# Optimization experiments

Hardware: AMD Instinct MI355X
Metric: run time of the kernel (lower is better)

Reference implementation:

```python
import jax, jax.numpy as jnp
import numpy as np
from jax import lax

RADIUS = 0.3
NSAMPLE = 16
NPOINT = 1024
NH = 1   # num_heading_bin
NS = 18  # num_size_cluster
EPS = 1e-5  # torch BatchNorm eps


def _bn(x, g, b, m, v):
    # eval-mode batchnorm over the last (channel) axis
    return (x - m) * (g / jnp.sqrt(v + EPS)) + b


def _fps(xyz, npoint):
    # furthest point sampling; xyz: (B,K,3) -> (B,npoint) int32 indices
    B, K, _ = xyz.shape
    def body(carry, _):
        dists, far = carry
        cur = jnp.take_along_axis(xyz, far[:, None, None], axis=1)  # (B,1,3)
        d = jnp.sum((xyz - cur) ** 2, -1)                           # (B,K)
        dists = jnp.minimum(dists, d)
        nxt = jnp.argmax(dists, -1).astype(jnp.int32)
        return (dists, nxt), far
    init = (jnp.full((B, K), 1e10, xyz.dtype), jnp.zeros((B,), jnp.int32))
    _, inds = lax.scan(body, init, None, length=npoint)
    return jnp.swapaxes(inds, 0, 1)  # (B, npoint)


def _ball_query(xyz, new_xyz):
    # first-NSAMPLE points within RADIUS of each center, pad with first hit
    K = xyz.shape[1]
    d2 = jnp.sum((new_xyz[:, :, None, :] - xyz[:, None, :, :]) ** 2, -1)  # (B,S,K)
    mask = d2 < RADIUS ** 2
    idx = jnp.where(mask, jnp.arange(K, dtype=jnp.int32)[None, None, :], K)
    idx = jnp.sort(idx, -1)[..., :NSAMPLE]
    first = idx[..., :1]
    idx = jnp.where(idx == K, first, idx)
    idx = jnp.where(idx == K, 0, idx)  # degenerate: no neighbor at all
    return idx  # (B,S,NSAMPLE)


def setup_inputs() -> dict:
    key = jax.random.key(0)
    ks = jax.random.split(key, 32)
    inp = {}
    inp['xyz'] = jax.random.normal(ks[0], (8, 8192, 3), jnp.float32)
    inp['features'] = jax.random.normal(ks[1], (8, 256, 8192), jnp.float32)
    i = 2
    # shared MLP: 259 -> 128 -> 128 -> 128 (conv2d 1x1, no bias, then BN)
    for l, (o, c) in enumerate([(128, 259), (128, 128), (128, 128)]):
        inp[f'mlp_w{l}'] = jax.random.normal(ks[i], (o, c), jnp.float32) * 0.1; i += 1
        inp[f'mlp_g{l}'] = jnp.ones((o,), jnp.float32)
        inp[f'mlp_b{l}'] = jnp.zeros((o,), jnp.float32)
        inp[f'mlp_m{l}'] = jax.random.normal(ks[i], (o,), jnp.float32) * 0.01; i += 1
        inp[f'mlp_v{l}'] = jax.random.uniform(ks[i], (o,), jnp.float32, 0.5, 1.5); i += 1
    # box head convs (conv1d k=1)
    for nm, (o, c) in [('c1', (128, 128)), ('c2', (128, 128)), ('c3', (97, 128))]:
        inp[f'{nm}_w'] = jax.random.normal(ks[i], (o, c), jnp.float32) * 0.1; i += 1
        inp[f'{nm}_b'] = jnp.zeros((o,), jnp.float32)
    for nm in ['bn1', 'bn2']:
        inp[f'{nm}_g'] = jnp.ones((128,), jnp.float32)
        inp[f'{nm}_b'] = jnp.zeros((128,), jnp.float32)
        inp[f'{nm}_m'] = jax.random.normal(ks[i], (128,), jnp.float32) * 0.01; i += 1
        inp[f'{nm}_v'] = jax.random.uniform(ks[i], (128,), jnp.float32, 0.5, 1.5); i += 1
    inp['mean_size_arr'] = jax.random.uniform(ks[i], (NS, 3), jnp.float32, 0.3, 2.0)
    return inp


def reference(xyz, features,
              mlp_w0, mlp_g0, mlp_b0, mlp_m0, mlp_v0,
              mlp_w1, mlp_g1, mlp_b1, mlp_m1, mlp_v1,
              mlp_w2, mlp_g2, mlp_b2, mlp_m2, mlp_v2,
              c1_w, c1_b, bn1_g, bn1_b, bn1_m, bn1_v,
              c2_w, c2_b, bn2_g, bn2_b, bn2_m, bn2_v,
              c3_w, c3_b, mean_size_arr):
    B = xyz.shape[0]
    # --- vote aggregation: FPS + ball query + group + shared MLP + maxpool ---
    fps_inds = _fps(xyz, NPOINT)
    new_xyz = jnp.take_along_axis(xyz, fps_inds[..., None], axis=1)  # (B,S,3)
    idx = _ball_query(xyz, new_xyz)                                  # (B,S,n)
    gather = jax.vmap(lambda a, i: a[i])
    g_xyz = (gather(xyz, idx) - new_xyz[:, :, None, :]) / RADIUS     # normalize_xyz
    g_f = gather(jnp.swapaxes(features, 1, 2), idx)                  # (B,S,n,256)
    h = jnp.concatenate([g_xyz, g_f], -1)                            # (B,S,n,259)
    for w, g, b, m, v in ((mlp_w0, mlp_g0, mlp_b0, mlp_m0, mlp_v0),
                          (mlp_w1, mlp_g1, mlp_b1, mlp_m1, mlp_v1),
                          (mlp_w2, mlp_g2, mlp_b2, mlp_m2, mlp_v2)):
        h = jax.nn.relu(_bn(jnp.einsum('bsnc,oc->bsno', h, w), g, b, m, v))
    feat = jnp.max(h, axis=2)                                        # (B,S,128)
    # --- box head (conv1d k=1 == per-point linear) ---
    net = jax.nn.relu(_bn(jnp.einsum('bsc,oc->bso', feat, c1_w) + c1_b,
                          bn1_g, bn1_b, bn1_m, bn1_v))
    net = jax.nn.relu(_bn(jnp.einsum('bsc,oc->bso', net, c2_w) + c2_b,
                          bn2_g, bn2_b, bn2_m, bn2_v))
    net = jnp.einsum('bsc,oc->bso', net, c3_w) + c3_b                # (B,S,97)
    # --- decode_scores ---
    obj = net[..., 0:2]
    center = new_xyz + net[..., 2:5]
    hs = net[..., 5:5 + NH]
    hr = net[..., 5 + NH:5 + 2 * NH] * (np.pi / NH)
    ss = net[..., 5 + 2 * NH:5 + 2 * NH + NS]
    srn = net[..., 5 + 2 * NH + NS:5 + 2 * NH + 4 * NS].reshape(B, NPOINT, NS, 3)
    sr = (srn * mean_size_arr[None, None]).reshape(B, NPOINT, NS * 3)
    sem = net[..., 5 + 2 * NH + 4 * NS:]
    return jnp.concatenate([obj, center, hs, hr, ss, sr, sem], -1)   # (B,S,97)
```

## Files before the change

### kernel.cpp

```cpp
#include <hip/hip_runtime.h>
#include <cstdint>
#include <cstddef>

#define BATCH   8
#define KPTS    8192
#define NPT     1024
#define NSAMP   16
#define RAD2    0.09f

typedef float f32x2 __attribute__((ext_vector_type(2)));
typedef float f32x4 __attribute__((ext_vector_type(4)));
typedef short s16x4 __attribute__((ext_vector_type(4)));
typedef short s16x8 __attribute__((ext_vector_type(8)));

__device__ __forceinline__ unsigned short f2bf(float x) {
    unsigned u = __float_as_uint(x);
    return (unsigned short)((u + 0x7fffu + ((u >> 16) & 1u)) >> 16);
}

template <int CTRL>
__device__ __forceinline__ float dppmaxf(float v) {
    int o = __builtin_amdgcn_update_dpp(0, __float_as_int(v), CTRL, 0xf, 0xf, true);
    return fmaxf(v, __int_as_float(o));
}

__global__ __launch_bounds__(256, 1) void fps_f0_kernel(
    const float* __restrict__ xyz, float* __restrict__ new_xyz,
    const float* __restrict__ feats, const float* __restrict__ w0,
    float* __restrict__ f0out) {
    __shared__ float xs[KPTS], ys[KPTS], zs[KPTS];
    __shared__ unsigned long long slot3[3];
    __shared__ int   hist[NPT];
    __shared__ float As[16 * 64];
    __shared__ float Bs[16 * 130];

    const int tid = threadIdx.x;

    if (blockIdx.x >= 8) {
        const int bid = blockIdx.x - 8;
        const int b   = bid >> 7;
        const int p0  = (bid & 127) << 6;
        const int rb  = (tid >> 4) << 2;
        const int ob  = tid & 15;
        const float* fb = feats + (size_t)b * 256 * KPTS;

        float acc[4][8];
#pragma unroll
        for (int r = 0; r < 4; ++r)
#pragma unroll
            for (int c = 0; c < 8; ++c) acc[r][c] = 0.f;

        for (int k0 = 0; k0 < 256; k0 += 16) {
#pragma unroll
            for (int i = 0; i < 4; ++i) {
                int e = tid + (i << 8);
                int kk = e >> 6, pc = e & 63;
                As[kk * 64 + pc] = fb[(size_t)(k0 + kk) * KPTS + p0 + pc];
            }
#pragma unroll
            for (int i = 0; i < 8; ++i) {
                int e = tid + (i << 8);
                int o = e >> 4, kk = e & 15;
                Bs[kk * 130 + o] = w0[o * 259 + 3 + k0 + kk];
            }
            __syncthreads();
#pragma unroll
            for (int kk = 0; kk < 16; ++kk) {
                float a[4], wvv[8];
#pragma unroll
                for (int r = 0; r < 4; ++r) a[r] = As[kk * 64 + rb + r];
#pragma unroll
                for (int c = 0; c < 8; ++c) wvv[c] = Bs[kk * 130 + ob + (c << 4)];
#pragma unroll
                for (int r = 0; r < 4; ++r)
#pragma unroll
                    for (int c = 0; c < 8; ++c) acc[r][c] = fmaf(a[r], wvv[c], acc[r][c]);
            }
            __syncthreads();
        }
#pragma unroll
        for (int r = 0; r < 4; ++r) {
            float* outp = f0out + ((size_t)b * KPTS + p0 + rb + r) * 128 + ob;
#pragma unroll
            for (int c = 0; c < 8; ++c) outp[c << 4] = acc[r][c];
        }
        return;
    }

    {
#pragma clang fp contract(off)
        const int b = blockIdx.x;
        const float* xb = xyz + (size_t)b * KPTS * 3;

        for (int i = tid; i < KPTS; i += 256) {
            xs[i] = xb[i * 3 + 0];
            ys[i] = xb[i * 3 + 1];
            zs[i] = xb[i * 3 + 2];
        }
        if (tid < 3) slot3[tid] = 0ull;
        __syncthreads();

        const int base = tid << 5;
        f32x2 px[16], py[16], pz[16], dmn[16];
#pragma unroll
        for (int j = 0; j < 16; ++j) {
            int i0 = base + (j << 1);
            px[j] = (f32x2){xs[i0], xs[i0 + 1]};
            py[j] = (f32x2){ys[i0], ys[i0 + 1]};
            pz[j] = (f32x2){zs[i0], zs[i0 + 1]};
            dmn[j] = (f32x2){1e10f, 1e10f};
        }

        const int lane = tid & 63;
        int far = 0;
        int cur = 0, nxt = 1;
        for (int it = 0; it < NPT; ++it) {
            if (tid == 0) { hist[it] = far; slot3[nxt] = 0ull; }
            const float cx = xs[far], cy = ys[far], cz = zs[far];
            const f32x2 cx2 = (f32x2){cx, cx};
            const f32x2 cy2 = (f32x2){cy, cy};
            const f32x2 cz2 = (f32x2){cz, cz};

            f32x2 mm = (f32x2){-1.0f, -1.0f};
#pragma unroll
            for (int j = 0; j < 16; ++j) {
                f32x2 dx = px[j] - cx2;
                f32x2 dy = py[j] - cy2;
                f32x2 dz = pz[j] - cz2;
                f32x2 d  = (dx * dx + dy * dy) + dz * dz;
                f32x2 nd = __builtin_elementwise_min(dmn[j], d);
                dmn[j] = nd;
                mm = __builtin_elementwise_max(mm, nd);
            }
            float lmax = fmaxf(mm.x, mm.y);

            int ci = 0x7fffffff;
#pragma unroll
            for (int j = 0; j < 16; ++j) {
                if (dmn[j].x == lmax) ci = min(ci, base + (j << 1));
                if (dmn[j].y == lmax) ci = min(ci, base + (j << 1) + 1);
            }

            float wm = lmax;
            wm = dppmaxf<0x111>(wm);
            wm = dppmaxf<0x112>(wm);
            wm = dppmaxf<0x114>(wm);
            wm = dppmaxf<0x118>(wm);
            wm = dppmaxf<0x142>(wm);
            wm = dppmaxf<0x143>(wm);
            float wmax = __int_as_float(
                __builtin_amdgcn_readlane(__float_as_int(wm), 63));

            unsigned long long mk = __ballot(lmax == wmax);
            int wl = (int)__builtin_ctzll(mk);
            int cw = __builtin_amdgcn_readlane(ci, wl);

            if (lane == 0) {
                unsigned long long pk =
                    ((unsigned long long)__float_as_uint(wmax) << 32)
                    | (unsigned)(8191 - cw);
                atomicMax(&slot3[cur], pk);
            }
            __syncthreads();

            unsigned long long g = slot3[cur];
            far = 8191 - (int)(unsigned)(g & 0xffffffffull);
            cur = nxt;
            nxt = (nxt == 2) ? 0 : nxt + 1;
        }

        for (int i = tid; i < NPT; i += 256) {
            int idx = hist[i];
            float* o = new_xyz + ((size_t)b * NPT + i) * 3;
            o[0] = xs[idx]; o[1] = ys[idx]; o[2] = zs[idx];
        }
    }
}

__global__ __launch_bounds__(256) void ballq_kernel(const float* __restrict__ xyz,
                                                    const float* __restrict__ new_xyz,
                                                    int* __restrict__ idxout) {
    const int tid  = threadIdx.x;
    const int lane = tid & 63;
    const int q    = (blockIdx.x << 2) + (tid >> 6);
    const int b    = q >> 10;
    const float* xb = xyz + (size_t)b * KPTS * 3;
    const float qx = new_xyz[q * 3 + 0];
    const float qy = new_xyz[q * 3 + 1];
    const float qz = new_xyz[q * 3 + 2];
    int* op = idxout + q * NSAMP;

    int total = 0;
    int first_p = 0;
    for (int c = 0; c < KPTS / 64; ++c) {
        int p = (c << 6) + lane;
        float pxv = xb[p * 3 + 0], pyv = xb[p * 3 + 1], pzv = xb[p * 3 + 2];
        float dx = __fsub_rn(qx, pxv), dy = __fsub_rn(qy, pyv), dz = __fsub_rn(qz, pzv);
        float d2 = __fadd_rn(__fadd_rn(__fmul_rn(dx, dx), __fmul_rn(dy, dy)),
                             __fmul_rn(dz, dz));
        bool pred = d2 < RAD2;
        unsigned long long mask = __ballot(pred);
        if (total == 0 && mask != 0ull) first_p = (c << 6) + (int)__builtin_ctzll(mask);
        if (pred) {
            int rank = (int)__popcll(mask & ((1ull << lane) - 1ull));
            int slot = total + rank;
            if (slot < NSAMP) op[slot] = p;
        }
        total += (int)__popcll(mask);
        if (total >= NSAMP) break;
    }
    if (total < NSAMP && lane >= total && lane < NSAMP) op[lane] = first_p;
}

#define HB 136

__global__ __launch_bounds__(256) void mlp_kernel(
    const float* __restrict__ f0, const int* __restrict__ idxw,
    const float* __restrict__ xyz, const float* __restrict__ new_xyz,
    const float* __restrict__ w0,
    const float* __restrict__ g0, const float* __restrict__ b0,
    const float* __restrict__ m0, const float* __restrict__ v0,
    const float* __restrict__ w1,
    const float* __restrict__ g1, const float* __restrict__ b1a,
    const float* __restrict__ m1, const float* __restrict__ v1,
    const float* __restrict__ w2,
    const float* __restrict__ g2, const float* __restrict__ b2a,
    const float* __restrict__ m2, const float* __restrict__ v2,
    float* __restrict__ featout) {
    const int tid = threadIdx.x;
    const int q0  = blockIdx.x << 2;
    const int b   = q0 >> 10;

    __shared__ __align__(16) unsigned short hbf[64 * HB];
    __shared__ __align__(16) unsigned short Wsh[128 * HB];
    __shared__ float gx[64], gy[64], gz[64];
    __shared__ int   pidx[64];
    __shared__ float s0[128], t0[128], wxs[128], wys[128], wzs[128];
    __shared__ float s1[128], t1[128], s2[128], t2[128];

    if (tid < 64) pidx[tid] = idxw[(q0 + (tid >> 4)) * NSAMP + (tid & 15)];
    if (tid < 128) {
        float sc = g0[tid] / sqrtf(v0[tid] + 1e-5f);
        s0[tid] = sc; t0[tid] = b0[tid] - m0[tid] * sc;
        sc = g1[tid] / sqrtf(v1[tid] + 1e-5f);
        s1[tid] = sc; t1[tid] = b1a[tid] - m1[tid] * sc;
        sc = g2[tid] / sqrtf(v2[tid] + 1e-5f);
        s2[tid] = sc; t2[tid] = b2a[tid] - m2[tid] * sc;
        wxs[tid] = w0[tid * 259 + 0];
        wys[tid] = w0[tid * 259 + 1];
        wzs[tid] = w0[tid * 259 + 2];
    }
    __syncthreads();
    if (tid < 64) {
        int p = pidx[tid];
        int q = q0 + (tid >> 4);
        const float* pp = xyz + ((size_t)b * KPTS + p) * 3;
        const float* nq = new_xyz + (size_t)q * 3;
        gx[tid] = (pp[0] - nq[0]) / 0.3f;
        gy[tid] = (pp[1] - nq[1]) / 0.3f;
        gz[tid] = (pp[2] - nq[2]) / 0.3f;
    }
    __syncthreads();

#pragma unroll 2
    for (int i = 0; i < 8; ++i) {
        int e = tid + (i << 8);
        int row = e >> 5, o = (e & 31) << 2;
        int p = pidx[row];
        float4 v4 = *(const float4*)(f0 + ((size_t)b * KPTS + p) * 128 + o);
        float gxr = gx[row], gyr = gy[row], gzr = gz[row];
        float r0 = fmaf(wzs[o + 0], gzr, fmaf(wys[o + 0], gyr, fmaf(wxs[o + 0], gxr, v4.x)));
        float r1 = fmaf(wzs[o + 1], gzr, fmaf(wys[o + 1], gyr, fmaf(wxs[o + 1], gxr, v4.y)));
        float r2 = fmaf(wzs[o + 2], gzr, fmaf(wys[o + 2], gyr, fmaf(wxs[o + 2], gxr, v4.z)));
        float r3 = fmaf(wzs[o + 3], gzr, fmaf(wys[o + 3], gyr, fmaf(wxs[o + 3], gxr, v4.w)));
        s16x4 c4;
        c4.x = (short)f2bf(fmaxf(fmaf(r0, s0[o + 0], t0[o + 0]), 0.f));
        c4.y = (short)f2bf(fmaxf(fmaf(r1, s0[o + 1], t0[o + 1]), 0.f));
        c4.z = (short)f2bf(fmaxf(fmaf(r2, s0[o + 2], t0[o + 2]), 0.f));
        c4.w = (short)f2bf(fmaxf(fmaf(r3, s0[o + 3], t0[o + 3]), 0.f));
        *(s16x4*)&hbf[row * HB + o] = c4;
    }
#pragma unroll 4
    for (int i = 0; i < 16; ++i) {
        int e = tid + (i << 8);
        int o = e >> 5;
        int kt = (e & 31) << 2;
        float4 w4 = *(const float4*)(w1 + o * 128 + kt);
        s16x4 c4 = { (short)f2bf(w4.x), (short)f2bf(w4.y),
                     (short)f2bf(w4.z), (short)f2bf(w4.w) };
        *(s16x4*)&Wsh[o * HB + kt] = c4;
    }
    __syncthreads();

    const int w    = tid >> 6;
    const int lane = tid & 63;
    const int l15  = lane & 15;
    const int quad = lane >> 4;
    const int wrow = w << 4;

    f32x4 acc[8];
#pragma unroll
    for (int t = 0; t < 8; ++t) acc[t] = (f32x4){0.f, 0.f, 0.f, 0.f};
#pragma unroll
    for (int k0 = 0; k0 < 128; k0 += 32) {
        s16x8 a = *(const s16x8*)&hbf[(wrow + l15) * HB + k0 + (quad << 3)];
#pragma unroll
        for (int t = 0; t < 8; ++t) {
            s16x8 bf = *(const s16x8*)&Wsh[((t << 4) + l15) * HB + k0 + (quad << 3)];
            acc[t] = __builtin_amdgcn_mfma_f32_16x16x32_bf16(a, bf, acc[t], 0, 0, 0);
        }
    }
    __syncthreads();

#pragma unroll
    for (int t = 0; t < 8; ++t) {
        int o = (t << 4) + l15;
        float ss = s1[o], tt = t1[o];
#pragma unroll
        for (int r = 0; r < 4; ++r) {
            float v = fmaxf(fmaf(acc[t][r], ss, tt), 0.f);
            hbf[(wrow + (quad << 2) + r) * HB + o] = f2bf(v);
        }
    }
#pragma unroll 4
    for (int i = 0; i < 16; ++i) {
        int e = tid + (i << 8);
        int o = e >> 5;
        int kt = (e & 31) << 2;
        float4 w4 = *(const float4*)(w2 + o * 128 + kt);
        s16x4 c4 = { (short)f2bf(w4.x), (short)f2bf(w4.y),
                     (short)f2bf(w4.z), (short)f2bf(w4.w) };
        *(s16x4*)&Wsh[o * HB + kt] = c4;
    }
    __syncthreads();

#pragma unroll
    for (int t = 0; t < 8; ++t) acc[t] = (f32x4){0.f, 0.f, 0.f, 0.f};
#pragma unroll
    for (int k0 = 0; k0 < 128; k0 += 32) {
        s16x8 a = *(const s16x8*)&hbf[(wrow + l15) * HB + k0 + (quad << 3)];
#pragma unroll
        for (int t = 0; t < 8; ++t) {
            s16x8 bf = *(const s16x8*)&Wsh[((t << 4) + l15) * HB + k0 + (quad << 3)];
            acc[t] = __builtin_amdgcn_mfma_f32_16x16x32_bf16(a, bf, acc[t], 0, 0, 0);
        }
    }

#pragma unroll
    for (int t = 0; t < 8; ++t) {
        int o = (t << 4) + l15;
        float ss = s2[o], tt = t2[o];
        float m0v = fmaxf(fmaf(acc[t][0], ss, tt), 0.f);
        float m1v = fmaxf(fmaf(acc[t][1], ss, tt), 0.f);
        float m2v = fmaxf(fmaf(acc[t][2], ss, tt), 0.f);
        float m3v = fmaxf(fmaf(acc[t][3], ss, tt), 0.f);
        float m = fmaxf(fmaxf(m0v, m1v), fmaxf(m2v, m3v));
        m = fmaxf(m, __shfl_xor(m, 16));
        m = fmaxf(m, __shfl_xor(m, 32));
        if (quad == 0)
            featout[(size_t)(q0 + w) * 128 + o] = m;
    }
}

__global__ __launch_bounds__(256) void head_kernel(
    const float* __restrict__ feat, const float* __restrict__ new_xyz,
    const float* __restrict__ c1w, const float* __restrict__ c1b,
    const float* __restrict__ c2w, const float* __restrict__ c2b,
    const float* __restrict__ c3w, const float* __restrict__ c3b,
    const float* __restrict__ bg1, const float* __restrict__ bb1,
    const float* __restrict__ bm1, const float* __restrict__ bv1,
    const float* __restrict__ bg2, const float* __restrict__ bb2,
    const float* __restrict__ bm2, const float* __restrict__ bv2,
    const float* __restrict__ msz, float* __restrict__ out) {
    const int tid = threadIdx.x;
    const int q0  = blockIdx.x << 3;
    __shared__ float fs[8][128], n1[8][128], n2[8][128];
    __shared__ float s1[128], t1[128], s2[128], t2[128], ms[54];

#pragma unroll
    for (int i = 0; i < 4; ++i) {
        int e = tid + (i << 8);
        fs[e >> 7][e & 127] = feat[(size_t)q0 * 128 + e];
    }
    if (tid < 128) {
        float sc = bg1[tid] / sqrtf(bv1[tid] + 1e-5f);
        s1[tid] = sc; t1[tid] = bb1[tid] - bm1[tid] * sc;
        sc = bg2[tid] / sqrtf(bv2[tid] + 1e-5f);
        s2[tid] = sc; t2[tid] = bb2[tid] - bm2[tid] * sc;
    }
    if (tid < 54) ms[tid] = msz[tid];
    __syncthreads();

    const int o    = tid & 127;
    const int half = tid >> 7;

    {
        float a[4];
#pragma unroll
        for (int j = 0; j < 4; ++j) a[j] = c1b[o];
        const float* wr = c1w + o * 128;
        for (int k = 0; k < 128; k += 4) {
            float4 w4 = *(const float4*)(wr + k);
#pragma unroll
            for (int j = 0; j < 4; ++j) {
                int qq = half * 4 + j;
                a[j] = fmaf(fs[qq][k + 0], w4.x, a[j]);
                a[j] = fmaf(fs[qq][k + 1], w4.y, a[j]);
                a[j] = fmaf(fs[qq][k + 2], w4.z, a[j]);
                a[j] = fmaf(fs[qq][k + 3], w4.w, a[j]);
            }
        }
#pragma unroll
        for (int j = 0; j < 4; ++j)
            n1[half * 4 + j][o] = fmaxf(fmaf(a[j], s1[o], t1[o]), 0.f);
    }
    __syncthreads();
    {
        float a[4];
#pragma unroll
        for (int j = 0; j < 4; ++j) a[j] = c2b[o];
        const float* wr = c2w + o * 128;
        for (int k = 0; k < 128; k += 4) {
            float4 w4 = *(const float4*)(wr + k);
#pragma unroll
            for (int j = 0; j < 4; ++j) {
                int qq = half * 4 + j;
                a[j] = fmaf(n1[qq][k + 0], w4.x, a[j]);
                a[j] = fmaf(n1[qq][k + 1], w4.y, a[j]);
                a[j] = fmaf(n1[qq][k + 2], w4.z, a[j]);
                a[j] = fmaf(n1[qq][k + 3], w4.w, a[j]);
            }
        }
#pragma unroll
        for (int j = 0; j < 4; ++j)
            n2[half * 4 + j][o] = fmaxf(fmaf(a[j], s2[o], t2[o]), 0.f);
    }
    __syncthreads();
    if (o < 97) {
        float a[4];
#pragma unroll
        for (int j = 0; j < 4; ++j) a[j] = c3b[o];
        const float* wr = c3w + o * 128;
        for (int k = 0; k < 128; k += 4) {
            float4 w4 = *(const float4*)(wr + k);
#pragma unroll
            for (int j = 0; j < 4; ++j) {
                int qq = half * 4 + j;
                a[j] = fmaf(n2[qq][k + 0], w4.x, a[j]);
                a[j] = fmaf(n2[qq][k + 1], w4.y, a[j]);
                a[j] = fmaf(n2[qq][k + 2], w4.z, a[j]);
                a[j] = fmaf(n2[qq][k + 3], w4.w, a[j]);
            }
        }
#pragma unroll
        for (int j = 0; j < 4; ++j) {
            int q = q0 + half * 4 + j;
            float v = a[j];
            if (o >= 2 && o < 5) v += new_xyz[(size_t)q * 3 + (o - 2)];
            else if (o == 6) v *= 3.14159265358979323846f;
            else if (o >= 25 && o < 79) v *= ms[o - 25];
            out[(size_t)q * 97 + o] = v;
        }
    }
}

extern "C" void kernel_launch(void* const* d_in, const int* in_sizes, int n_in,
                              void* d_out, int out_size, void* d_ws, size_t ws_size,
                              hipStream_t stream) {
    const float* xyz      = (const float*)d_in[0];
    const float* features = (const float*)d_in[1];
    const float* w0  = (const float*)d_in[2];
    const float* g0  = (const float*)d_in[3];
    const float* b0  = (const float*)d_in[4];
    const float* m0  = (const float*)d_in[5];
    const float* v0  = (const float*)d_in[6];
    const float* w1  = (const float*)d_in[7];
    const float* g1  = (const float*)d_in[8];
    const float* b1  = (const float*)d_in[9];
    const float* m1  = (const float*)d_in[10];
    const float* v1  = (const float*)d_in[11];
    const float* w2  = (const float*)d_in[12];
    const float* g2  = (const float*)d_in[13];
    const float* b2  = (const float*)d_in[14];
    const float* m2  = (const float*)d_in[15];
    const float* v2  = (const float*)d_in[16];
    const float* c1w = (const float*)d_in[17];
    const float* c1b = (const float*)d_in[18];
    const float* c2w = (const float*)d_in[19];
    const float* c2b = (const float*)d_in[20];
    const float* c3w = (const float*)d_in[21];
    const float* c3b = (const float*)d_in[22];
    const float* bg1 = (const float*)d_in[23];
    const float* bb1 = (const float*)d_in[24];
    const float* bm1 = (const float*)d_in[25];
    const float* bv1 = (const float*)d_in[26];
    const float* bg2 = (const float*)d_in[27];
    const float* bb2 = (const float*)d_in[28];
    const float* bm2 = (const float*)d_in[29];
    const float* bv2 = (const float*)d_in[30];
    const float* msz = (const float*)d_in[31];

    float* F0   = (float*)d_ws;
    float* feat = F0 + (size_t)BATCH * KPTS * 128;
    int*   idxw = (int*)(feat + (size_t)BATCH * NPT * 128);
    float* nxyz = (float*)(idxw + (size_t)BATCH * NPT * NSAMP);
    float* outp = (float*)d_out;

    fps_f0_kernel<<<8 + BATCH * (KPTS / 64), 256, 0, stream>>>(
        xyz, nxyz, features, w0, F0);
    ballq_kernel<<<BATCH * NPT / 4, 256, 0, stream>>>(xyz, nxyz, idxw);
    mlp_kernel  <<<BATCH * NPT / 4, 256, 0, stream>>>(
        F0, idxw, xyz, nxyz, w0, g0, b0, m0, v0,
        w1, g1, b1, m1, v1, w2, g2, b2, m2, v2, feat);
    head_kernel <<<BATCH * NPT / 8, 256, 0, stream>>>(
        feat, nxyz, c1w, c1b, c2w, c2b, c3w, c3b,
        bg1, bb1, bm1, bv1, bg2, bb2, bm2, bv2, msz, outp);
}
```

Baseline: 1.233 ms.

## Fuse FPS, feature GEMM, ball query and MLP into persistent kernel with counters

Merges the FPS, first-layer feature GEMM, ball query and shared-MLP kernels into one persistent kernel of 256 blocks. Eight blocks run FPS and publish sampled centers in chunks of 32 through global atomic counters. The other 248 blocks first compute the feature GEMM, then start ball query and MLP for each group of centers as soon as those centers are published. This overlaps the serial FPS with the MLP work and removes kernel-launch gaps and the ball-query index round trip through memory. The cost is spin-wait polling, a shared-memory union, and reliance on all 256 blocks being resident at once to avoid deadlock.

```diff
diff --git a/kernel.cpp b/kernel.cpp
--- a/kernel.cpp
+++ b/kernel.cpp
@@ -7,6 +7,8 @@
 #define NPT     1024
 #define NSAMP   16
 #define RAD2    0.09f
+#define HB      136
+#define NWORK   248
 
 typedef float f32x2 __attribute__((ext_vector_type(2)));
 typedef float f32x4 __attribute__((ext_vector_type(4)));
@@ -24,80 +26,62 @@
     return fmaxf(v, __int_as_float(o));
 }
 
-__global__ __launch_bounds__(256, 1) void fps_f0_kernel(
+__device__ __forceinline__ int aload(int* p) {
+    return __hip_atomic_load(p, __ATOMIC_ACQUIRE, __HIP_MEMORY_SCOPE_AGENT);
+}
+__device__ __forceinline__ void abump(int* p, int v) {
+    __hip_atomic_fetch_add(p, v, __ATOMIC_RELEASE, __HIP_MEMORY_SCOPE_AGENT);
+}
+
+union __align__(16) SM {
+    struct {
+        float xs[KPTS], ys[KPTS], zs[KPTS];
+        unsigned long long slot3[3];
+        int hist[NPT];
+    } fps;
+    struct {
+        float As[16 * 64];
+        float Bs[16 * 130];
+    } gemm;
+    struct {
+        unsigned short W1[128 * HB];
+        unsigned short W2[128 * HB];
+        unsigned short hbf[64 * HB];
+        float gx[64], gy[64], gz[64];
+        int   pidx[64];
+        float s0[128], t0[128], wxs[128], wys[128], wzs[128];
+        float s1[128], t1[128], s2[128], t2[128];
+    } mlp;
+};
+
+__global__ __launch_bounds__(256, 1) void mega_kernel(
     const float* __restrict__ xyz, float* __restrict__ new_xyz,
     const float* __restrict__ feats, const float* __restrict__ w0,
-    float* __restrict__ f0out) {
-    __shared__ float xs[KPTS], ys[KPTS], zs[KPTS];
-    __shared__ unsigned long long slot3[3];
-    __shared__ int   hist[NPT];
-    __shared__ float As[16 * 64];
-    __shared__ float Bs[16 * 130];
-
+    float* __restrict__ f0out,
+    const float* __restrict__ g0, const float* __restrict__ b0,
+    const float* __restrict__ m0, const float* __restrict__ v0,
+    const float* __restrict__ w1,
+    const float* __restrict__ g1, const float* __restrict__ b1a,
+    const float* __restrict__ m1, const float* __restrict__ v1,
+    const float* __restrict__ w2,
+    const float* __restrict__ g2, const float* __restrict__ b2a,
+    const float* __restrict__ m2, const float* __restrict__ v2,
+    float* __restrict__ featout, int* __restrict__ cnt) {
+    __shared__ SM sm;
     const int tid = threadIdx.x;
-
-    if (blockIdx.x >= 8) {
-        const int bid = blockIdx.x - 8;
-        const int b   = bid >> 7;
-        const int p0  = (bid & 127) << 6;
-        const int rb  = (tid >> 4) << 2;
-        const int ob  = tid & 15;
-        const float* fb = feats + (size_t)b * 256 * KPTS;
-
-        float acc[4][8];
-#pragma unroll
-        for (int r = 0; r < 4; ++r)
-#pragma unroll
-            for (int c = 0; c < 8; ++c) acc[r][c] = 0.f;
-
-        for (int k0 = 0; k0 < 256; k0 += 16) {
-#pragma unroll
-            for (int i = 0; i < 4; ++i) {
-                int e = tid + (i << 8);
-                int kk = e >> 6, pc = e & 63;
-                As[kk * 64 + pc] = fb[(size_t)(k0 + kk) * KPTS + p0 + pc];
-            }
-#pragma unroll
-            for (int i = 0; i < 8; ++i) {
-                int e = tid + (i << 8);
-                int o = e >> 4, kk = e & 15;
-                Bs[kk * 130 + o] = w0[o * 259 + 3 + k0 + kk];
-            }
-            __syncthreads();
-#pragma unroll
-            for (int kk = 0; kk < 16; ++kk) {
-                float a[4], wvv[8];
-#pragma unroll
-                for (int r = 0; r < 4; ++r) a[r] = As[kk * 64 + rb + r];
-#pragma unroll
-                for (int c = 0; c < 8; ++c) wvv[c] = Bs[kk * 130 + ob + (c << 4)];
-#pragma unroll
-                for (int r = 0; r < 4; ++r)
-#pragma unroll
-                    for (int c = 0; c < 8; ++c) acc[r][c] = fmaf(a[r], wvv[c], acc[r][c]);
-            }
-            __syncthreads();
-        }
-#pragma unroll
-        for (int r = 0; r < 4; ++r) {
-            float* outp = f0out + ((size_t)b * KPTS + p0 + rb + r) * 128 + ob;
-#pragma unroll
-            for (int c = 0; c < 8; ++c) outp[c << 4] = acc[r][c];
-        }
-        return;
-    }
-
-    {
+    const int bid = blockIdx.x;
+
+    if (bid < 8) {
 #pragma clang fp contract(off)
-        const int b = blockIdx.x;
+        const int b = bid;
         const float* xb = xyz + (size_t)b * KPTS * 3;
 
         for (int i = tid; i < KPTS; i += 256) {
-            xs[i] = xb[i * 3 + 0];
-            ys[i] = xb[i * 3 + 1];
-            zs[i] = xb[i * 3 + 2];
-        }
-        if (tid < 3) slot3[tid] = 0ull;
+            sm.fps.xs[i] = xb[i * 3 + 0];
+            sm.fps.ys[i] = xb[i * 3 + 1];
+            sm.fps.zs[i] = xb[i * 3 + 2];
+        }
+        if (tid < 3) sm.fps.slot3[tid] = 0ull;
         __syncthreads();
 
         const int base = tid << 5;
@@ -105,9 +89,9 @@
 #pragma unroll
         for (int j = 0; j < 16; ++j) {
             int i0 = base + (j << 1);
-            px[j] = (f32x2){xs[i0], xs[i0 + 1]};
-            py[j] = (f32x2){ys[i0], ys[i0 + 1]};
-            pz[j] = (f32x2){zs[i0], zs[i0 + 1]};
+            px[j] = (f32x2){sm.fps.xs[i0], sm.fps.xs[i0 + 1]};
+            py[j] = (f32x2){sm.fps.ys[i0], sm.fps.ys[i0 + 1]};
+            pz[j] = (f32x2){sm.fps.zs[i0], sm.fps.zs[i0 + 1]};
             dmn[j] = (f32x2){1e10f, 1e10f};
         }
 
@@ -115,8 +99,8 @@
         int far = 0;
         int cur = 0, nxt = 1;
         for (int it = 0; it < NPT; ++it) {
-            if (tid == 0) { hist[it] = far; slot3[nxt] = 0ull; }
-            const float cx = xs[far], cy = ys[far], cz = zs[far];
+            if (tid == 0) { sm.fps.hist[it] = far; sm.fps.slot3[nxt] = 0ull; }
+            const float cx = sm.fps.xs[far], cy = sm.fps.ys[far], cz = sm.fps.zs[far];
             const f32x2 cx2 = (f32x2){cx, cx};
             const f32x2 cy2 = (f32x2){cy, cy};
             const f32x2 cz2 = (f32x2){cz, cz};
@@ -159,206 +143,249 @@
                 unsigned long long pk =
                     ((unsigned long long)__float_as_uint(wmax) << 32)
                     | (unsigned)(8191 - cw);
-                atomicMax(&slot3[cur], pk);
+                atomicMax(&sm.fps.slot3[cur], pk);
             }
             __syncthreads();
 
-            unsigned long long g = slot3[cur];
+            unsigned long long g = sm.fps.slot3[cur];
             far = 8191 - (int)(unsigned)(g & 0xffffffffull);
             cur = nxt;
             nxt = (nxt == 2) ? 0 : nxt + 1;
-        }
-
-        for (int i = tid; i < NPT; i += 256) {
-            int idx = hist[i];
-            float* o = new_xyz + ((size_t)b * NPT + i) * 3;
-            o[0] = xs[idx]; o[1] = ys[idx]; o[2] = zs[idx];
-        }
-    }
-}
-
-__global__ __launch_bounds__(256) void ballq_kernel(const float* __restrict__ xyz,
-                                                    const float* __restrict__ new_xyz,
-                                                    int* __restrict__ idxout) {
-    const int tid  = threadIdx.x;
-    const int lane = tid & 63;
-    const int q    = (blockIdx.x << 2) + (tid >> 6);
-    const int b    = q >> 10;
-    const float* xb = xyz + (size_t)b * KPTS * 3;
-    const float qx = new_xyz[q * 3 + 0];
-    const float qy = new_xyz[q * 3 + 1];
-    const float qz = new_xyz[q * 3 + 2];
-    int* op = idxout + q * NSAMP;
-
-    int total = 0;
-    int first_p = 0;
-    for (int c = 0; c < KPTS / 64; ++c) {
-        int p = (c << 6) + lane;
-        float pxv = xb[p * 3 + 0], pyv = xb[p * 3 + 1], pzv = xb[p * 3 + 2];
-        float dx = __fsub_rn(qx, pxv), dy = __fsub_rn(qy, pyv), dz = __fsub_rn(qz, pzv);
-        float d2 = __fadd_rn(__fadd_rn(__fmul_rn(dx, dx), __fmul_rn(dy, dy)),
-                             __fmul_rn(dz, dz));
-        bool pred = d2 < RAD2;
-        unsigned long long mask = __ballot(pred);
-        if (total == 0 && mask != 0ull) first_p = (c << 6) + (int)__builtin_ctzll(mask);
-        if (pred) {
-            int rank = (int)__popcll(mask & ((1ull << lane) - 1ull));
-            int slot = total + rank;
-            if (slot < NSAMP) op[slot] = p;
-        }
-        total += (int)__popcll(mask);
-        if (total >= NSAMP) break;
-    }
-    if (total < NSAMP && lane >= total && lane < NSAMP) op[lane] = first_p;
-}
-
-#define HB 136
-
-__global__ __launch_bounds__(256) void mlp_kernel(
-    const float* __restrict__ f0, const int* __restrict__ idxw,
-    const float* __restrict__ xyz, const float* __restrict__ new_xyz,
-    const float* __restrict__ w0,
-    const float* __restrict__ g0, const float* __restrict__ b0,
-    const float* __restrict__ m0, const float* __restrict__ v0,
-    const float* __restrict__ w1,
-    const float* __restrict__ g1, const float* __restrict__ b1a,
-    const float* __restrict__ m1, const float* __restrict__ v1,
-    const float* __restrict__ w2,
-    const float* __restrict__ g2, const float* __restrict__ b2a,
-    const float* __restrict__ m2, const float* __restrict__ v2,
-    float* __restrict__ featout) {
-    const int tid = threadIdx.x;
-    const int q0  = blockIdx.x << 2;
-    const int b   = q0 >> 10;
-
-    __shared__ __align__(16) unsigned short hbf[64 * HB];
-    __shared__ __align__(16) unsigned short Wsh[128 * HB];
-    __shared__ float gx[64], gy[64], gz[64];
-    __shared__ int   pidx[64];
-    __shared__ float s0[128], t0[128], wxs[128], wys[128], wzs[128];
-    __shared__ float s1[128], t1[128], s2[128], t2[128];
-
-    if (tid < 64) pidx[tid] = idxw[(q0 + (tid >> 4)) * NSAMP + (tid & 15)];
+
+            if ((it & 31) == 31) {
+                if (tid < 128) {
+                    int c = tid & 3;
+                    if (c < 3) {
+                        int i = (it - 31) + (tid >> 2);
+                        int idx = sm.fps.hist[i];
+                        float v = (c == 0) ? sm.fps.xs[idx]
+                                 : (c == 1) ? sm.fps.ys[idx] : sm.fps.zs[idx];
+                        new_xyz[((size_t)b * NPT + i) * 3 + c] = v;
+                    }
+                }
+                __threadfence();
+                __syncthreads();
+                if (tid == 0) abump(&cnt[b], 32);
+            }
+        }
+        return;
+    }
+
+    const int wk = bid - 8;
+
+    {
+        const int rb = (tid >> 4) << 2;
+        const int ob = tid & 15;
+        for (int t = wk; t < 1024; t += NWORK) {
+            const int b  = t >> 7;
+            const int p0 = (t & 127) << 6;
+            const float* fb = feats + (size_t)b * 256 * KPTS;
+
+            float acc[4][8];
+#pragma unroll
+            for (int r = 0; r < 4; ++r)
+#pragma unroll
+                for (int c = 0; c < 8; ++c) acc[r][c] = 0.f;
+
+            for (int k0 = 0; k0 < 256; k0 += 16) {
+#pragma unroll
+                for (int i = 0; i < 4; ++i) {
+                    int e = tid + (i << 8);
+                    int kk = e >> 6, pc = e & 63;
+                    sm.gemm.As[kk * 64 + pc] = fb[(size_t)(k0 + kk) * KPTS + p0 + pc];
+                }
+#pragma unroll
+                for (int i = 0; i < 8; ++i) {
+                    int e = tid + (i << 8);
+                    int o = e >> 4, kk = e & 15;
+                    sm.gemm.Bs[kk * 130 + o] = w0[o * 259 + 3 + k0 + kk];
+                }
+                __syncthreads();
+#pragma unroll
+                for (int kk = 0; kk < 16; ++kk) {
+                    float a[4], wvv[8];
+#pragma unroll
+                    for (int r = 0; r < 4; ++r) a[r] = sm.gemm.As[kk * 64 + rb + r];
+#pragma unroll
+                    for (int c = 0; c < 8; ++c) wvv[c] = sm.gemm.Bs[kk * 130 + ob + (c << 4)];
+#pragma unroll
+                    for (int r = 0; r < 4; ++r)
+#pragma unroll
+                        for (int c = 0; c < 8; ++c) acc[r][c] = fmaf(a[r], wvv[c], acc[r][c]);
+                }
+                __syncthreads();
+            }
+#pragma unroll
+            for (int r = 0; r < 4; ++r) {
+                float* outp = f0out + ((size_t)b * KPTS + p0 + rb + r) * 128 + ob;
+#pragma unroll
+                for (int c = 0; c < 8; ++c) outp[c << 4] = acc[r][c];
+            }
+        }
+        __threadfence();
+        __syncthreads();
+        if (tid == 0) abump(&cnt[8], 1);
+    }
+
     if (tid < 128) {
         float sc = g0[tid] / sqrtf(v0[tid] + 1e-5f);
-        s0[tid] = sc; t0[tid] = b0[tid] - m0[tid] * sc;
+        sm.mlp.s0[tid] = sc; sm.mlp.t0[tid] = b0[tid] - m0[tid] * sc;
         sc = g1[tid] / sqrtf(v1[tid] + 1e-5f);
-        s1[tid] = sc; t1[tid] = b1a[tid] - m1[tid] * sc;
+        sm.mlp.s1[tid] = sc; sm.mlp.t1[tid] = b1a[tid] - m1[tid] * sc;
         sc = g2[tid] / sqrtf(v2[tid] + 1e-5f);
-        s2[tid] = sc; t2[tid] = b2a[tid] - m2[tid] * sc;
-        wxs[tid] = w0[tid * 259 + 0];
-        wys[tid] = w0[tid * 259 + 1];
-        wzs[tid] = w0[tid * 259 + 2];
-    }
-    __syncthreads();
-    if (tid < 64) {
-        int p = pidx[tid];
-        int q = q0 + (tid >> 4);
-        const float* pp = xyz + ((size_t)b * KPTS + p) * 3;
-        const float* nq = new_xyz + (size_t)q * 3;
-        gx[tid] = (pp[0] - nq[0]) / 0.3f;
-        gy[tid] = (pp[1] - nq[1]) / 0.3f;
-        gz[tid] = (pp[2] - nq[2]) / 0.3f;
-    }
-    __syncthreads();
-
-#pragma unroll 2
-    for (int i = 0; i < 8; ++i) {
-        int e = tid + (i << 8);
-        int row = e >> 5, o = (e & 31) << 2;
-        int p = pidx[row];
-        float4 v4 = *(const float4*)(f0 + ((size_t)b * KPTS + p) * 128 + o);
-        float gxr = gx[row], gyr = gy[row], gzr = gz[row];
-        float r0 = fmaf(wzs[o + 0], gzr, fmaf(wys[o + 0], gyr, fmaf(wxs[o + 0], gxr, v4.x)));
-        float r1 = fmaf(wzs[o + 1], gzr, fmaf(wys[o + 1], gyr, fmaf(wxs[o + 1], gxr, v4.y)));
-        float r2 = fmaf(wzs[o + 2], gzr, fmaf(wys[o + 2], gyr, fmaf(wxs[o + 2], gxr, v4.z)));
-        float r3 = fmaf(wzs[o + 3], gzr, fmaf(wys[o + 3], gyr, fmaf(wxs[o + 3], gxr, v4.w)));
-        s16x4 c4;
-        c4.x = (short)f2bf(fmaxf(fmaf(r0, s0[o + 0], t0[o + 0]), 0.f));
-        c4.y = (short)f2bf(fmaxf(fmaf(r1, s0[o + 1], t0[o + 1]), 0.f));
-        c4.z = (short)f2bf(fmaxf(fmaf(r2, s0[o + 2], t0[o + 2]), 0.f));
-        c4.w = (short)f2bf(fmaxf(fmaf(r3, s0[o + 3], t0[o + 3]), 0.f));
-        *(s16x4*)&hbf[row * HB + o] = c4;
+        sm.mlp.s2[tid] = sc; sm.mlp.t2[tid] = b2a[tid] - m2[tid] * sc;
+        sm.mlp.wxs[tid] = w0[tid * 259 + 0];
+        sm.mlp.wys[tid] = w0[tid * 259 + 1];
+        sm.mlp.wzs[tid] = w0[tid * 259 + 2];
     }
 #pragma unroll 4
     for (int i = 0; i < 16; ++i) {
         int e = tid + (i << 8);
         int o = e >> 5;
         int kt = (e & 31) << 2;
-        float4 w4 = *(const float4*)(w1 + o * 128 + kt);
-        s16x4 c4 = { (short)f2bf(w4.x), (short)f2bf(w4.y),
-                     (short)f2bf(w4.z), (short)f2bf(w4.w) };
-        *(s16x4*)&Wsh[o * HB + kt] = c4;
+        float4 a4 = *(const float4*)(w1 + o * 128 + kt);
+        s16x4 c4 = { (short)f2bf(a4.x), (short)f2bf(a4.y),
+                     (short)f2bf(a4.z), (short)f2bf(a4.w) };
+        *(s16x4*)&sm.mlp.W1[o * HB + kt] = c4;
+        float4 b4 = *(const float4*)(w2 + o * 128 + kt);
+        s16x4 d4 = { (short)f2bf(b4.x), (short)f2bf(b4.y),
+                     (short)f2bf(b4.z), (short)f2bf(b4.w) };
+        *(s16x4*)&sm.mlp.W2[o * HB + kt] = d4;
     }
     __syncthreads();
 
+    const int lane = tid & 63;
     const int w    = tid >> 6;
-    const int lane = tid & 63;
     const int l15  = lane & 15;
     const int quad = lane >> 4;
     const int wrow = w << 4;
 
-    f32x4 acc[8];
-#pragma unroll
-    for (int t = 0; t < 8; ++t) acc[t] = (f32x4){0.f, 0.f, 0.f, 0.f};
-#pragma unroll
-    for (int k0 = 0; k0 < 128; k0 += 32) {
-        s16x8 a = *(const s16x8*)&hbf[(wrow + l15) * HB + k0 + (quad << 3)];
+    for (int g = wk; g < 2048; g += NWORK) {
+        const int b  = g & 7;
+        const int qg = g >> 3;
+        const int q0 = (b << 10) + (qg << 2);
+
+        if (tid == 0) {
+            while (aload(&cnt[8]) < NWORK) __builtin_amdgcn_s_sleep(16);
+            const int need = (qg << 2) + 4;
+            while (aload(&cnt[b]) < need) __builtin_amdgcn_s_sleep(16);
+        }
+        __syncthreads();
+
+        {
+            const int q = q0 + w;
+            const float* xb = xyz + (size_t)b * KPTS * 3;
+            const float qx = new_xyz[q * 3 + 0];
+            const float qy = new_xyz[q * 3 + 1];
+            const float qz = new_xyz[q * 3 + 2];
+            int* op = &sm.mlp.pidx[w << 4];
+
+            int total = 0;
+            int first_p = 0;
+            for (int c = 0; c < KPTS / 64; ++c) {
+                int p = (c << 6) + lane;
+                float pxv = xb[p * 3 + 0], pyv = xb[p * 3 + 1], pzv = xb[p * 3 + 2];
+                float dx = __fsub_rn(qx, pxv), dy = __fsub_rn(qy, pyv), dz = __fsub_rn(qz, pzv);
+                float d2 = __fadd_rn(__fadd_rn(__fmul_rn(dx, dx), __fmul_rn(dy, dy)),
+                                     __fmul_rn(dz, dz));
+                bool pred = d2 < RAD2;
+                unsigned long long mask = __ballot(pred);
+                if (total == 0 && mask != 0ull) first_p = (c << 6) + (int)__builtin_ctzll(mask);
+                if (pred) {
+                    int rank = (int)__popcll(mask & ((1ull << lane) - 1ull));
+                    int slot = total + rank;
+                    if (slot < NSAMP) op[slot] = p;
+                }
+                total += (int)__popcll(mask);
+                if (total >= NSAMP) break;
+            }
+            if (total < NSAMP && lane >= total && lane < NSAMP) op[lane] = first_p;
+        }
+        __syncthreads();
+
+        if (tid < 64) {
+            int p = sm.mlp.pidx[tid];
+            int q = q0 + (tid >> 4);
+            const float* pp = xyz + ((size_t)b * KPTS + p) * 3;
+            const float* nq = new_xyz + (size_t)q * 3;
+            sm.mlp.gx[tid] = (pp[0] - nq[0]) / 0.3f;
+            sm.mlp.gy[tid] = (pp[1] - nq[1]) / 0.3f;
+            sm.mlp.gz[tid] = (pp[2] - nq[2]) / 0.3f;
+        }
+        __syncthreads();
+
+#pragma unroll 2
+        for (int i = 0; i < 8; ++i) {
+            int e = tid + (i << 8);
+            int row = e >> 5, o = (e & 31) << 2;
+            int p = sm.mlp.pidx[row];
+            float4 v4 = *(const float4*)(f0out + ((size_t)b * KPTS + p) * 128 + o);
+            float gxr = sm.mlp.gx[row], gyr = sm.mlp.gy[row], gzr = sm.mlp.gz[row];
+            float r0 = fmaf(sm.mlp.wzs[o + 0], gzr, fmaf(sm.mlp.wys[o + 0], gyr, fmaf(sm.mlp.wxs[o + 0], gxr, v4.x)));
+            float r1 = fmaf(sm.mlp.wzs[o + 1], gzr, fmaf(sm.mlp.wys[o + 1], gyr, fmaf(sm.mlp.wxs[o + 1], gxr, v4.y)));
+            float r2 = fmaf(sm.mlp.wzs[o + 2], gzr, fmaf(sm.mlp.wys[o + 2], gyr, fmaf(sm.mlp.wxs[o + 2], gxr, v4.z)));
+            float r3 = fmaf(sm.mlp.wzs[o + 3], gzr, fmaf(sm.mlp.wys[o + 3], gyr, fmaf(sm.mlp.wxs[o + 3], gxr, v4.w)));
+            s16x4 c4;
+            c4.x = (short)f2bf(fmaxf(fmaf(r0, sm.mlp.s0[o + 0], sm.mlp.t0[o + 0]), 0.f));
+            c4.y = (short)f2bf(fmaxf(fmaf(r1, sm.mlp.s0[o + 1], sm.mlp.t0[o + 1]), 0.f));
+            c4.z = (short)f2bf(fmaxf(fmaf(r2, sm.mlp.s0[o + 2], sm.mlp.t0[o + 2]), 0.f));
+            c4.w = (short)f2bf(fmaxf(fmaf(r3, sm.mlp.s0[o + 3], sm.mlp.t0[o + 3]), 0.f));
+            *(s16x4*)&sm.mlp.hbf[row * HB + o] = c4;
+        }
+        __syncthreads();
+
+        f32x4 acc[8];
+#pragma unroll
+        for (int t = 0; t < 8; ++t) acc[t] = (f32x4){0.f, 0.f, 0.f, 0.f};
+#pragma unroll
+        for (int k0 = 0; k0 < 128; k0 += 32) {
+            s16x8 a = *(const s16x8*)&sm.mlp.hbf[(wrow + l15) * HB + k0 + (quad << 3)];
+#pragma unroll
+            for (int t = 0; t < 8; ++t) {
+                s16x8 bf = *(const s16x8*)&sm.mlp.W1[((t << 4) + l15) * HB + k0 + (quad << 3)];
+                acc[t] = __builtin_amdgcn_mfma_f32_16x16x32_bf16(a, bf, acc[t], 0, 0, 0);
+            }
+        }
+        __syncthreads();
+
 #pragma unroll
         for (int t = 0; t < 8; ++t) {
-            s16x8 bf = *(const s16x8*)&Wsh[((t << 4) + l15) * HB + k0 + (quad << 3)];
-            acc[t] = __builtin_amdgcn_mfma_f32_16x16x32_bf16(a, bf, acc[t], 0, 0, 0);
-        }
-    }
-    __syncthreads();
-
-#pragma unroll
-    for (int t = 0; t < 8; ++t) {
-        int o = (t << 4) + l15;
-        float ss = s1[o], tt = t1[o];
-#pragma unroll
-        for (int r = 0; r < 4; ++r) {
-            float v = fmaxf(fmaf(acc[t][r], ss, tt), 0.f);
-            hbf[(wrow + (quad << 2) + r) * HB + o] = f2bf(v);
-        }
-    }
-#pragma unroll 4
-    for (int i = 0; i < 16; ++i) {
-        int e = tid + (i << 8);
-        int o = e >> 5;
-        int kt = (e & 31) << 2;
-        float4 w4 = *(const float4*)(w2 + o * 128 + kt);
-        s16x4 c4 = { (short)f2bf(w4.x), (short)f2bf(w4.y),
-                     (short)f2bf(w4.z), (short)f2bf(w4.w) };
-        *(s16x4*)&Wsh[o * HB + kt] = c4;
-    }
-    __syncthreads();
-
-#pragma unroll
-    for (int t = 0; t < 8; ++t) acc[t] = (f32x4){0.f, 0.f, 0.f, 0.f};
-#pragma unroll
-    for (int k0 = 0; k0 < 128; k0 += 32) {
-        s16x8 a = *(const s16x8*)&hbf[(wrow + l15) * HB + k0 + (quad << 3)];
+            int o = (t << 4) + l15;
+            float ss = sm.mlp.s1[o], tt = sm.mlp.t1[o];
+#pragma unroll
+            for (int r = 0; r < 4; ++r) {
+                float v = fmaxf(fmaf(acc[t][r], ss, tt), 0.f);
+                sm.mlp.hbf[(wrow + (quad << 2) + r) * HB + o] = f2bf(v);
+            }
+        }
+        __syncthreads();
+
+#pragma unroll
+        for (int t = 0; t < 8; ++t) acc[t] = (f32x4){0.f, 0.f, 0.f, 0.f};
+#pragma unroll
+        for (int k0 = 0; k0 < 128; k0 += 32) {
+            s16x8 a = *(const s16x8*)&sm.mlp.hbf[(wrow + l15) * HB + k0 + (quad << 3)];
+#pragma unroll
+            for (int t = 0; t < 8; ++t) {
+                s16x8 bf = *(const s16x8*)&sm.mlp.W2[((t << 4) + l15) * HB + k0 + (quad << 3)];
+                acc[t] = __builtin_amdgcn_mfma_f32_16x16x32_bf16(a, bf, acc[t], 0, 0, 0);
+            }
+        }
+
 #pragma unroll
         for (int t = 0; t < 8; ++t) {
-            s16x8 bf = *(const s16x8*)&Wsh[((t << 4) + l15) * HB + k0 + (quad << 3)];
-            acc[t] = __builtin_amdgcn_mfma_f32_16x16x32_bf16(a, bf, acc[t], 0, 0, 0);
-        }
-    }
-
-#pragma unroll
-    for (int t = 0; t < 8; ++t) {
-        int o = (t << 4) + l15;
-        float ss = s2[o], tt = t2[o];
-        float m0v = fmaxf(fmaf(acc[t][0], ss, tt), 0.f);
-        float m1v = fmaxf(fmaf(acc[t][1], ss, tt), 0.f);
-        float m2v = fmaxf(fmaf(acc[t][2], ss, tt), 0.f);
-        float m3v = fmaxf(fmaf(acc[t][3], ss, tt), 0.f);
-        float m = fmaxf(fmaxf(m0v, m1v), fmaxf(m2v, m3v));
-        m = fmaxf(m, __shfl_xor(m, 16));
-        m = fmaxf(m, __shfl_xor(m, 32));
-        if (quad == 0)
-            featout[(size_t)(q0 + w) * 128 + o] = m;
+            int o = (t << 4) + l15;
+            float ss = sm.mlp.s2[o], tt = sm.mlp.t2[o];
+            float m0v = fmaxf(fmaf(acc[t][0], ss, tt), 0.f);
+            float m1v = fmaxf(fmaf(acc[t][1], ss, tt), 0.f);
+            float m2v = fmaxf(fmaf(acc[t][2], ss, tt), 0.f);
+            float m3v = fmaxf(fmaf(acc[t][3], ss, tt), 0.f);
+            float m = fmaxf(fmaxf(m0v, m1v), fmaxf(m2v, m3v));
+            m = fmaxf(m, __shfl_xor(m, 16));
+            m = fmaxf(m, __shfl_xor(m, 32));
+            if (quad == 0)
+                featout[(size_t)(q0 + w) * 128 + o] = m;
+        }
     }
 }
 
@@ -502,16 +529,15 @@
 
     float* F0   = (float*)d_ws;
     float* feat = F0 + (size_t)BATCH * KPTS * 128;
-    int*   idxw = (int*)(feat + (size_t)BATCH * NPT * 128);
-    float* nxyz = (float*)(idxw + (size_t)BATCH * NPT * NSAMP);
+    int*   cnt  = (int*)(feat + (size_t)BATCH * NPT * 128);
+    float* nxyz = (float*)(cnt + (size_t)BATCH * NPT * NSAMP);
     float* outp = (float*)d_out;
 
-    fps_f0_kernel<<<8 + BATCH * (KPTS / 64), 256, 0, stream>>>(
-        xyz, nxyz, features, w0, F0);
-    ballq_kernel<<<BATCH * NPT / 4, 256, 0, stream>>>(xyz, nxyz, idxw);
-    mlp_kernel  <<<BATCH * NPT / 4, 256, 0, stream>>>(
-        F0, idxw, xyz, nxyz, w0, g0, b0, m0, v0,
-        w1, g1, b1, m1, v1, w2, g2, b2, m2, v2, feat);
+    hipMemsetAsync(cnt, 0, 16 * sizeof(int), stream);
+    mega_kernel<<<256, 256, 0, stream>>>(
+        xyz, nxyz, features, w0, F0,
+        g0, b0, m0, v0, w1, g1, b1, m1, v1, w2, g2, b2, m2, v2,
+        feat, cnt);
     head_kernel <<<BATCH * NPT / 8, 256, 0, stream>>>(
         feat, nxyz, c1w, c1b, c2w, c2b, c3w, c3b,
         bg1, bb1, bm1, bv1, bg2, bb2, bm2, bv2, msz, outp);
```

After: 1.259 ms. 2.1% more time.
